# Kernel optimization log

Hardware: AMD Instinct MI355X
Metric: run time of the kernel (lower is better)

## Reference

```python
import jax, jax.numpy as jnp
import numpy as np

DIM = 192
HEADS = 6
WS = 7
N = WS * WS  # 49
B_ = 4096
NW = 64


def _relative_position_index(ws):
    coords = np.stack(np.meshgrid(np.arange(ws), np.arange(ws), indexing='ij'))  # (2, ws, ws)
    cf = coords.reshape(2, -1)  # (2, N)
    rel = cf[:, :, None] - cf[:, None, :]  # (2, N, N)
    rel = rel.transpose(1, 2, 0).copy()
    rel[:, :, 0] += ws - 1
    rel[:, :, 1] += ws - 1
    rel[:, :, 0] *= 2 * ws - 1
    return jnp.asarray(rel.sum(-1), dtype=jnp.int32)  # (N, N)


def setup_inputs() -> dict:
    key = jax.random.key(0)
    ks = jax.random.split(key, 8)
    x = jax.random.normal(ks[0], (B_, N, DIM), dtype=jnp.float32)
    mask = jax.random.normal(ks[1], (NW, N, N), dtype=jnp.float32)
    qkv_w = jax.random.normal(ks[2], (3 * DIM, DIM), dtype=jnp.float32) * 0.02
    qkv_b = jnp.zeros((3 * DIM,), dtype=jnp.float32)
    proj_w = jax.random.normal(ks[3], (DIM, DIM), dtype=jnp.float32) * 0.02
    proj_b = jnp.zeros((DIM,), dtype=jnp.float32)
    n_bias = (2 * WS - 1) * (2 * WS - 1)  # 169
    bias_table = jax.random.truncated_normal(ks[4], -2.0, 2.0, (n_bias, HEADS), dtype=jnp.float32) * 0.02
    rel_idx = _relative_position_index(WS)
    return {"x": x, "mask": mask, "qkv_w": qkv_w, "qkv_b": qkv_b,
            "proj_w": proj_w, "proj_b": proj_b, "bias_table": bias_table,
            "rel_idx": rel_idx}


def reference(x, mask, qkv_w, qkv_b, proj_w, proj_b, bias_table, rel_idx):
    Bw, n, c = x.shape
    hd = c // HEADS
    scale = hd ** -0.5
    qkv = x @ qkv_w.T + qkv_b  # (B_, N, 3C)
    qkv = qkv.reshape(Bw, n, 3, HEADS, hd).transpose(2, 0, 3, 1, 4)  # (3, B_, H, N, hd)
    q, k, v = qkv[0] * scale, qkv[1], qkv[2]
    attn = jnp.einsum('bhqd,bhkd->bhqk', q, k)  # (B_, H, N, N)
    bias = bias_table[rel_idx.reshape(-1)].reshape(n, n, HEADS).transpose(2, 0, 1)  # (H, N, N)
    attn = attn + bias[None]
    nW = mask.shape[0]
    attn = attn.reshape(Bw // nW, nW, HEADS, n, n) + mask[None, :, None]
    attn = jax.nn.softmax(attn.reshape(Bw, HEADS, n, n), axis=-1)
    out = jnp.einsum('bhqk,bhkd->bhqd', attn, v)  # (B_, H, N, hd)
    out = out.transpose(0, 2, 1, 3).reshape(Bw, n, c)
    return out @ proj_w.T + proj_b
```

## Files before the change

### kernel.cpp

```cpp
#include <hip/hip_runtime.h>
#include <hip/hip_fp16.h>


typedef short bf16x8 __attribute__((ext_vector_type(8)));
typedef float f32x4 __attribute__((ext_vector_type(4)));

#define MFMA16(a, b, c) __builtin_amdgcn_mfma_f32_16x16x32_bf16((a), (b), (c), 0, 0, 0)

#define DIMC 192
#define NTOK 49

__device__ __forceinline__ unsigned short f2bf(float f) {
  unsigned int u = __float_as_uint(f);
  u += 0x7fffu + ((u >> 16) & 1u);
  return (unsigned short)(u >> 16);
}

__device__ __forceinline__ unsigned int cvt_pk_bf16(float lo, float hi) {
  unsigned int r;
  asm("v_cvt_pk_bf16_f32 %0, %1, %2" : "=v"(r) : "v"(lo), "v"(hi));
  return r;
}

__global__ void prep_kernel(const float* __restrict__ qkv_w,
                            const float* __restrict__ proj_w,
                            const float* __restrict__ bias_table,
                            const int* __restrict__ rel_idx,
                            const float* __restrict__ mask,
                            unsigned short* __restrict__ qkv_wb,
                            unsigned short* __restrict__ proj_wb,
                            __half* __restrict__ bmT) {
  int i = blockIdx.x * 256 + threadIdx.x;
  if (i < 576 * 192) qkv_wb[i] = f2bf(qkv_w[i]);
  if (i < 192 * 192) proj_wb[i] = f2bf(proj_w[i]);
  {
    int r = i & 3;
    int q = (i >> 2) & 63;
    int lq = (i >> 8) & 3;
    int nt = (i >> 10) & 3;
    int hw = i >> 12;
    int h = hw % 6;
    int widx = hw / 6;
    int k = nt * 16 + lq * 4 + r;
    float v;
    if (k >= NTOK) v = -30000.f;
    else if (q >= NTOK) v = 0.f;
    else v = bias_table[rel_idx[q * NTOK + k] * 6 + h] +
             mask[(size_t)widx * (NTOK * NTOK) + q * NTOK + k];
    bmT[i] = __float2half(v);
  }
}

__global__ __launch_bounds__(256, 2) void winattn_kernel(
    const float* __restrict__ x,
    const float* __restrict__ qkv_b,
    const float* __restrict__ proj_b,
    const unsigned short* __restrict__ qkv_wb,
    const unsigned short* __restrict__ proj_wb,
    const __half* __restrict__ bmT,
    float* __restrict__ out) {
  __shared__ unsigned short pool[39424];
  unsigned short* xb   = pool;
  unsigned short* Qall = pool;
  unsigned short* Kall = pool + 12800;
  unsigned short* Vta  = pool + 25600;

  const int tid = threadIdx.x;
  const int b = blockIdx.x;
  const int widx = b & 63;
  const int lane = tid & 63;
  const int wv = tid >> 6;
  const int lq = lane >> 4;
  const int ln = lane & 15;

  {
    const float4* xp = (const float4*)(x + (size_t)b * (NTOK * DIMC));
    for (int i = tid; i < NTOK * DIMC / 4; i += 256) {
      float4 v = xp[i];
      int fl = i * 4;
      int r = fl / DIMC;
      int c = fl - r * DIMC;
      unsigned int lo = (unsigned int)f2bf(v.x) | ((unsigned int)f2bf(v.y) << 16);
      unsigned int hi = (unsigned int)f2bf(v.z) | ((unsigned int)f2bf(v.w) << 16);
      *(uint2*)(&xb[r * 200 + c]) = make_uint2(lo, hi);
    }
    for (int i = tid; i < 15 * 200 / 2; i += 256)
      ((unsigned int*)(&xb[49 * 200]))[i] = 0u;
  }
  __syncthreads();

  bf16x8 af[4][6];
#pragma unroll
  for (int mt = 0; mt < 4; ++mt)
#pragma unroll
    for (int ks = 0; ks < 6; ++ks)
      af[mt][ks] = *(const bf16x8*)&xb[(mt * 16 + ln) * 200 + ks * 32 + lq * 8];
  __syncthreads();

  const float scale = 0.17677669529663687f;

  for (int i = 0; i < 9; ++i) {
    int nt = wv * 9 + i;
    int c = nt * 16 + ln;
    const unsigned short* wp = qkv_wb + (size_t)c * DIMC + lq * 8;
    bf16x8 wf[6];
#pragma unroll
    for (int ks = 0; ks < 6; ++ks) wf[ks] = *(const bf16x8*)(wp + ks * 32);
    float bv = qkv_b[c];
    f32x4 a0 = (f32x4){bv, bv, bv, bv};
    f32x4 a1 = a0, a2 = a0, a3 = a0;
#pragma unroll
    for (int ks = 0; ks < 6; ++ks) {
      a0 = MFMA16(af[0][ks], wf[ks], a0);
      a1 = MFMA16(af[1][ks], wf[ks], a1);
      a2 = MFMA16(af[2][ks], wf[ks], a2);
      a3 = MFMA16(af[3][ks], wf[ks], a3);
    }
    f32x4 acc[4] = {a0, a1, a2, a3};
    int which = nt / 12;
    int colq = c - which * 192;
    if (which == 0) {
#pragma unroll
      for (int mt = 0; mt < 4; ++mt) {
        int row0 = mt * 16 + lq * 4;
#pragma unroll
        for (int r = 0; r < 4; ++r)
          Qall[(row0 + r) * 200 + colq] = f2bf(acc[mt][r] * scale);
      }
    } else if (which == 1) {
#pragma unroll
      for (int mt = 0; mt < 4; ++mt) {
        int row0 = mt * 16 + lq * 4;
#pragma unroll
        for (int r = 0; r < 4; ++r)
          Kall[(row0 + r) * 200 + colq] = f2bf(acc[mt][r]);
      }
    } else {
#pragma unroll
      for (int mt = 0; mt < 4; ++mt) {
        int row0 = mt * 16 + lq * 4;
        unsigned int lo = cvt_pk_bf16(acc[mt][0], acc[mt][1]);
        unsigned int hi = cvt_pk_bf16(acc[mt][2], acc[mt][3]);
        *(uint2*)(&Vta[colq * 72 + row0]) = make_uint2(lo, hi);
      }
    }
  }
  __syncthreads();

  f32x4 pacc[12];
#pragma unroll
  for (int nti = 0; nti < 12; ++nti) {
    float pbv = proj_b[nti * 16 + ln];
    pacc[nti] = (f32x4){pbv, pbv, pbv, pbv};
  }

  const __half* bmp = bmT + (size_t)widx * 6 * 4096;
  const int sA = ((lq & 1) << 5) | ln;
  const int sB = sA + 16;
  const int hiSel = lq >> 1;

  for (int h = 0; h < 6; ++h) {
    uint2 bmu[4];
    {
      const __half* bmh = bmp + (size_t)h * 4096;
#pragma unroll
      for (int nt = 0; nt < 4; ++nt)
        bmu[nt] = *(const uint2*)(bmh + ((nt * 4 + lq) * 64 + wv * 16 + ln) * 4);
    }

    bf16x8 qf = *(const bf16x8*)&Qall[(wv * 16 + ln) * 200 + h * 32 + lq * 8];
    f32x4 sv[4];
#pragma unroll
    for (int nt = 0; nt < 4; ++nt) {
      bf16x8 kf = *(const bf16x8*)&Kall[(nt * 16 + ln) * 200 + h * 32 + lq * 8];
      sv[nt] = MFMA16(kf, qf, ((f32x4){0.f, 0.f, 0.f, 0.f}));
    }
    float tt[4][4];
#pragma unroll
    for (int nt = 0; nt < 4; ++nt) {
      float2 f01 = __half22float2(*(const __half2*)&bmu[nt].x);
      float2 f23 = __half22float2(*(const __half2*)&bmu[nt].y);
      tt[nt][0] = sv[nt][0] + f01.x;
      tt[nt][1] = sv[nt][1] + f01.y;
      tt[nt][2] = sv[nt][2] + f23.x;
      tt[nt][3] = sv[nt][3] + f23.y;
    }
    float m = tt[0][0];
#pragma unroll
    for (int nt = 0; nt < 4; ++nt)
#pragma unroll
      for (int r = 0; r < 4; ++r) m = fmaxf(m, tt[nt][r]);
    m = fmaxf(m, __shfl_xor(m, 16, 64));
    m = fmaxf(m, __shfl_xor(m, 32, 64));
    float sum = 0.f;
#pragma unroll
    for (int nt = 0; nt < 4; ++nt)
#pragma unroll
      for (int r = 0; r < 4; ++r) {
        float e = __expf(tt[nt][r] - m);
        tt[nt][r] = e;
        sum += e;
      }
    sum += __shfl_xor(sum, 16, 64);
    sum += __shfl_xor(sum, 32, 64);
    float pinv = 1.f / sum;

    unsigned int pk[4][2];
#pragma unroll
    for (int nt = 0; nt < 4; ++nt) {
      pk[nt][0] = cvt_pk_bf16(tt[nt][0], tt[nt][1]);
      pk[nt][1] = cvt_pk_bf16(tt[nt][2], tt[nt][3]);
    }
    union U8 { unsigned int u[4]; bf16x8 v; };
    U8 pb0, pb1;
#pragma unroll
    for (int w = 0; w < 4; ++w) {
      int src = (w & 2) ? sB : sA;
      int a0 = __shfl((int)pk[0][w & 1], src, 64);
      int a1 = __shfl((int)pk[1][w & 1], src, 64);
      int b0 = __shfl((int)pk[2][w & 1], src, 64);
      int b1 = __shfl((int)pk[3][w & 1], src, 64);
      pb0.u[w] = (unsigned int)(hiSel ? a1 : a0);
      pb1.u[w] = (unsigned int)(hiSel ? b1 : b0);
    }
    f32x4 o[2];
#pragma unroll
    for (int db = 0; db < 2; ++db) {
      bf16x8 v0 = *(const bf16x8*)&Vta[(h * 32 + db * 16 + ln) * 72 + lq * 8];
      bf16x8 v1 = *(const bf16x8*)&Vta[(h * 32 + db * 16 + ln) * 72 + 32 + lq * 8];
      f32x4 acc = (f32x4){0.f, 0.f, 0.f, 0.f};
      acc = MFMA16(v0, pb0.v, acc);
      acc = MFMA16(v1, pb1.v, acc);
      o[db] = acc;
    }
    unsigned int pkO[2][2];
#pragma unroll
    for (int db = 0; db < 2; ++db) {
      pkO[db][0] = cvt_pk_bf16(o[db][0] * pinv, o[db][1] * pinv);
      pkO[db][1] = cvt_pk_bf16(o[db][2] * pinv, o[db][3] * pinv);
    }
    U8 oa;
#pragma unroll
    for (int w = 0; w < 4; ++w) {
      int src = (w & 2) ? sB : sA;
      int a0 = __shfl((int)pkO[0][w & 1], src, 64);
      int a1 = __shfl((int)pkO[1][w & 1], src, 64);
      oa.u[w] = (unsigned int)(hiSel ? a1 : a0);
    }
#pragma unroll
    for (int nti = 0; nti < 12; ++nti) {
      bf16x8 w = *(const bf16x8*)(proj_wb + (size_t)(nti * 16 + ln) * DIMC + h * 32 + lq * 8);
      pacc[nti] = MFMA16(oa.v, w, pacc[nti]);
    }
  }

  {
    float* outp = out + (size_t)b * (NTOK * DIMC);
#pragma unroll
    for (int nti = 0; nti < 12; ++nti) {
      int col = nti * 16 + ln;
#pragma unroll
      for (int r = 0; r < 4; ++r) {
        int row = wv * 16 + lq * 4 + r;
        if (row < NTOK) outp[row * DIMC + col] = pacc[nti][r];
      }
    }
  }
}

extern "C" void kernel_launch(void* const* d_in, const int* in_sizes, int n_in,
                              void* d_out, int out_size, void* d_ws, size_t ws_size,
                              hipStream_t stream) {
  const float* x = (const float*)d_in[0];
  const float* mask = (const float*)d_in[1];
  const float* qkv_w = (const float*)d_in[2];
  const float* qkv_b = (const float*)d_in[3];
  const float* proj_w = (const float*)d_in[4];
  const float* proj_b = (const float*)d_in[5];
  const float* bias_table = (const float*)d_in[6];
  const int* rel_idx = (const int*)d_in[7];

  unsigned short* qkv_wb = (unsigned short*)d_ws;
  unsigned short* proj_wb = qkv_wb + 576 * 192;
  __half* bmT = (__half*)(proj_wb + 192 * 192);

  prep_kernel<<<6144, 256, 0, stream>>>(qkv_w, proj_w, bias_table, rel_idx,
                                        mask, qkv_wb, proj_wb, bmT);
  winattn_kernel<<<4096, 256, 0, stream>>>(x, qkv_b, proj_b,
                                           qkv_wb, proj_wb, bmT,
                                           (float*)d_out);
}
```

Before: 528.3 us.

## Split heads across 8 waves, keep Q in registers, use exp2 softmax

Doubles the block to 512 threads (8 waves). Each pair of waves shares a 16-row strip and splits the six heads three and three, and the two partial projection results are combined through shared memory before the store. Q is computed per wave straight into MFMA operand registers, which removes the Q buffer from LDS and cuts shared memory per block. Softmax uses exp2 with log2e folded into the Q scale and the precomputed bias/mask. The aim is more parallelism and occupancy, at the cost of an extra reduction through LDS, an extra barrier and more register pressure.

```diff
diff --git a/kernel.cpp b/kernel.cpp
--- a/kernel.cpp
+++ b/kernel.cpp
@@ -30,6 +30,7 @@
                             unsigned short* __restrict__ qkv_wb,
                             unsigned short* __restrict__ proj_wb,
                             __half* __restrict__ bmT) {
+  const float LOG2E = 1.4426950408889634f;
   int i = blockIdx.x * 256 + threadIdx.x;
   if (i < 576 * 192) qkv_wb[i] = f2bf(qkv_w[i]);
   if (i < 192 * 192) proj_wb[i] = f2bf(proj_w[i]);
@@ -43,15 +44,15 @@
     int widx = hw / 6;
     int k = nt * 16 + lq * 4 + r;
     float v;
-    if (k >= NTOK) v = -30000.f;
+    if (k >= NTOK) v = -30000.f * LOG2E;
     else if (q >= NTOK) v = 0.f;
-    else v = bias_table[rel_idx[q * NTOK + k] * 6 + h] +
-             mask[(size_t)widx * (NTOK * NTOK) + q * NTOK + k];
+    else v = (bias_table[rel_idx[q * NTOK + k] * 6 + h] +
+              mask[(size_t)widx * (NTOK * NTOK) + q * NTOK + k]) * LOG2E;
     bmT[i] = __float2half(v);
   }
 }
 
-__global__ __launch_bounds__(256, 2) void winattn_kernel(
+__global__ __launch_bounds__(512, 6) void winattn_kernel(
     const float* __restrict__ x,
     const float* __restrict__ qkv_b,
     const float* __restrict__ proj_b,
@@ -59,11 +60,11 @@
     const unsigned short* __restrict__ proj_wb,
     const __half* __restrict__ bmT,
     float* __restrict__ out) {
-  __shared__ unsigned short pool[39424];
+  __shared__ unsigned short pool[26624];
   unsigned short* xb   = pool;
-  unsigned short* Qall = pool;
-  unsigned short* Kall = pool + 12800;
-  unsigned short* Vta  = pool + 25600;
+  unsigned short* Kall = pool;
+  unsigned short* Vta  = pool + 12800;
+  float* scr = (float*)pool;
 
   const int tid = threadIdx.x;
   const int b = blockIdx.x;
@@ -72,10 +73,12 @@
   const int wv = tid >> 6;
   const int lq = lane >> 4;
   const int ln = lane & 15;
+  const int strip = wv >> 1;
+  const int hsel = wv & 1;
 
   {
     const float4* xp = (const float4*)(x + (size_t)b * (NTOK * DIMC));
-    for (int i = tid; i < NTOK * DIMC / 4; i += 256) {
+    for (int i = tid; i < NTOK * DIMC / 4; i += 512) {
       float4 v = xp[i];
       int fl = i * 4;
       int r = fl / DIMC;
@@ -84,7 +87,7 @@
       unsigned int hi = (unsigned int)f2bf(v.z) | ((unsigned int)f2bf(v.w) << 16);
       *(uint2*)(&xb[r * 200 + c]) = make_uint2(lo, hi);
     }
-    for (int i = tid; i < 15 * 200 / 2; i += 256)
+    for (int i = tid; i < 15 * 200 / 2; i += 512)
       ((unsigned int*)(&xb[49 * 200]))[i] = 0u;
   }
   __syncthreads();
@@ -95,18 +98,54 @@
 #pragma unroll
     for (int ks = 0; ks < 6; ++ks)
       af[mt][ks] = *(const bf16x8*)&xb[(mt * 16 + ln) * 200 + ks * 32 + lq * 8];
-  __syncthreads();
-
-  const float scale = 0.17677669529663687f;
-
-  for (int i = 0; i < 9; ++i) {
-    int nt = wv * 9 + i;
-    int c = nt * 16 + ln;
-    const unsigned short* wp = qkv_wb + (size_t)c * DIMC + lq * 8;
+  bf16x8 afs[6];
+#pragma unroll
+  for (int ks = 0; ks < 6; ++ks)
+    afs[ks] = *(const bf16x8*)&xb[(strip * 16 + ln) * 200 + ks * 32 + lq * 8];
+  __syncthreads();
+
+  const float scale2 = 0.17677669529663687f * 1.4426950408889634f;
+  const int sA = ((lq & 1) << 5) | ln;
+  const int sB = sA + 16;
+  const int hiSel = lq >> 1;
+  union U8 { unsigned int u[4]; bf16x8 v; };
+
+  unsigned int pkQ[6][2];
+  const int dbase = hsel * 96;
+#pragma unroll
+  for (int ct = 0; ct < 6; ++ct) {
+    const unsigned short* wp = qkv_wb + (size_t)(dbase + ct * 16 + ln) * DIMC + lq * 8;
     bf16x8 wf[6];
 #pragma unroll
     for (int ks = 0; ks < 6; ++ks) wf[ks] = *(const bf16x8*)(wp + ks * 32);
-    float bv = qkv_b[c];
+    float4 bq = *(const float4*)&qkv_b[dbase + ct * 16 + lq * 4];
+    f32x4 acc = (f32x4){bq.x, bq.y, bq.z, bq.w};
+#pragma unroll
+    for (int ks = 0; ks < 6; ++ks) acc = MFMA16(wf[ks], afs[ks], acc);
+    pkQ[ct][0] = cvt_pk_bf16(acc[0] * scale2, acc[1] * scale2);
+    pkQ[ct][1] = cvt_pk_bf16(acc[2] * scale2, acc[3] * scale2);
+  }
+  U8 qb[3];
+#pragma unroll
+  for (int hh = 0; hh < 3; ++hh)
+#pragma unroll
+    for (int w = 0; w < 4; ++w) {
+      int src = (w & 2) ? sB : sA;
+      int a0 = __shfl((int)pkQ[2 * hh][w & 1], src, 64);
+      int a1 = __shfl((int)pkQ[2 * hh + 1][w & 1], src, 64);
+      qb[hh].u[w] = (unsigned int)(hiSel ? a1 : a0);
+    }
+
+  for (int i = 0; i < 3; ++i) {
+    int t = wv * 3 + i;
+    int isK = (t < 12);
+    int colt = isK ? t : (t - 12);
+    int row = (isK ? 192 : 384) + colt * 16 + ln;
+    const unsigned short* wp = qkv_wb + (size_t)row * DIMC + lq * 8;
+    bf16x8 wf[6];
+#pragma unroll
+    for (int ks = 0; ks < 6; ++ks) wf[ks] = *(const bf16x8*)(wp + ks * 32);
+    float bv = qkv_b[row];
     f32x4 a0 = (f32x4){bv, bv, bv, bv};
     f32x4 a1 = a0, a2 = a0, a3 = a0;
 #pragma unroll
@@ -117,23 +156,14 @@
       a3 = MFMA16(af[3][ks], wf[ks], a3);
     }
     f32x4 acc[4] = {a0, a1, a2, a3};
-    int which = nt / 12;
-    int colq = c - which * 192;
-    if (which == 0) {
+    int db = colt * 16 + ln;
+    if (isK) {
 #pragma unroll
       for (int mt = 0; mt < 4; ++mt) {
         int row0 = mt * 16 + lq * 4;
 #pragma unroll
         for (int r = 0; r < 4; ++r)
-          Qall[(row0 + r) * 200 + colq] = f2bf(acc[mt][r] * scale);
-      }
-    } else if (which == 1) {
-#pragma unroll
-      for (int mt = 0; mt < 4; ++mt) {
-        int row0 = mt * 16 + lq * 4;
-#pragma unroll
-        for (int r = 0; r < 4; ++r)
-          Kall[(row0 + r) * 200 + colq] = f2bf(acc[mt][r]);
+          Kall[(row0 + r) * 200 + db] = f2bf(acc[mt][r]);
       }
     } else {
 #pragma unroll
@@ -141,7 +171,7 @@
         int row0 = mt * 16 + lq * 4;
         unsigned int lo = cvt_pk_bf16(acc[mt][0], acc[mt][1]);
         unsigned int hi = cvt_pk_bf16(acc[mt][2], acc[mt][3]);
-        *(uint2*)(&Vta[colq * 72 + row0]) = make_uint2(lo, hi);
+        *(uint2*)(&Vta[db * 72 + row0]) = make_uint2(lo, hi);
       }
     }
   }
@@ -150,30 +180,27 @@
   f32x4 pacc[12];
 #pragma unroll
   for (int nti = 0; nti < 12; ++nti) {
-    float pbv = proj_b[nti * 16 + ln];
+    float pbv = hsel ? 0.f : proj_b[nti * 16 + ln];
     pacc[nti] = (f32x4){pbv, pbv, pbv, pbv};
   }
 
   const __half* bmp = bmT + (size_t)widx * 6 * 4096;
-  const int sA = ((lq & 1) << 5) | ln;
-  const int sB = sA + 16;
-  const int hiSel = lq >> 1;
-
-  for (int h = 0; h < 6; ++h) {
+
+  for (int hh = 0; hh < 3; ++hh) {
+    const int h = hsel * 3 + hh;
     uint2 bmu[4];
     {
       const __half* bmh = bmp + (size_t)h * 4096;
 #pragma unroll
       for (int nt = 0; nt < 4; ++nt)
-        bmu[nt] = *(const uint2*)(bmh + ((nt * 4 + lq) * 64 + wv * 16 + ln) * 4);
-    }
-
-    bf16x8 qf = *(const bf16x8*)&Qall[(wv * 16 + ln) * 200 + h * 32 + lq * 8];
+        bmu[nt] = *(const uint2*)(bmh + ((nt * 4 + lq) * 64 + strip * 16 + ln) * 4);
+    }
+
     f32x4 sv[4];
 #pragma unroll
     for (int nt = 0; nt < 4; ++nt) {
       bf16x8 kf = *(const bf16x8*)&Kall[(nt * 16 + ln) * 200 + h * 32 + lq * 8];
-      sv[nt] = MFMA16(kf, qf, ((f32x4){0.f, 0.f, 0.f, 0.f}));
+      sv[nt] = MFMA16(kf, qb[hh].v, ((f32x4){0.f, 0.f, 0.f, 0.f}));
     }
     float tt[4][4];
 #pragma unroll
@@ -185,22 +212,24 @@
       tt[nt][2] = sv[nt][2] + f23.x;
       tt[nt][3] = sv[nt][3] + f23.y;
     }
-    float m = tt[0][0];
-#pragma unroll
-    for (int nt = 0; nt < 4; ++nt)
-#pragma unroll
-      for (int r = 0; r < 4; ++r) m = fmaxf(m, tt[nt][r]);
+    float m0 = fmaxf(fmaxf(tt[0][0], tt[0][1]), fmaxf(tt[0][2], tt[0][3]));
+    float m1 = fmaxf(fmaxf(tt[1][0], tt[1][1]), fmaxf(tt[1][2], tt[1][3]));
+    float m2 = fmaxf(fmaxf(tt[2][0], tt[2][1]), fmaxf(tt[2][2], tt[2][3]));
+    float m3 = fmaxf(fmaxf(tt[3][0], tt[3][1]), fmaxf(tt[3][2], tt[3][3]));
+    float m = fmaxf(fmaxf(m0, m1), fmaxf(m2, m3));
     m = fmaxf(m, __shfl_xor(m, 16, 64));
     m = fmaxf(m, __shfl_xor(m, 32, 64));
-    float sum = 0.f;
-#pragma unroll
-    for (int nt = 0; nt < 4; ++nt)
-#pragma unroll
-      for (int r = 0; r < 4; ++r) {
-        float e = __expf(tt[nt][r] - m);
-        tt[nt][r] = e;
-        sum += e;
-      }
+    float s[4];
+#pragma unroll
+    for (int nt = 0; nt < 4; ++nt) {
+      float e0 = exp2f(tt[nt][0] - m);
+      float e1 = exp2f(tt[nt][1] - m);
+      float e2 = exp2f(tt[nt][2] - m);
+      float e3 = exp2f(tt[nt][3] - m);
+      tt[nt][0] = e0; tt[nt][1] = e1; tt[nt][2] = e2; tt[nt][3] = e3;
+      s[nt] = (e0 + e1) + (e2 + e3);
+    }
+    float sum = (s[0] + s[1]) + (s[2] + s[3]);
     sum += __shfl_xor(sum, 16, 64);
     sum += __shfl_xor(sum, 32, 64);
     float pinv = 1.f / sum;
@@ -211,7 +240,6 @@
       pk[nt][0] = cvt_pk_bf16(tt[nt][0], tt[nt][1]);
       pk[nt][1] = cvt_pk_bf16(tt[nt][2], tt[nt][3]);
     }
-    union U8 { unsigned int u[4]; bf16x8 v; };
     U8 pb0, pb1;
 #pragma unroll
     for (int w = 0; w < 4; ++w) {
@@ -249,20 +277,33 @@
     }
 #pragma unroll
     for (int nti = 0; nti < 12; ++nti) {
-      bf16x8 w = *(const bf16x8*)(proj_wb + (size_t)(nti * 16 + ln) * DIMC + h * 32 + lq * 8);
+      bf16x8 w = *(const bf16x8*)(proj_wb +
+          (size_t)(nti * 16 + ln) * DIMC + h * 32 + lq * 8);
       pacc[nti] = MFMA16(oa.v, w, pacc[nti]);
     }
   }
 
-  {
+  __syncthreads();
+  if (hsel) {
+    float* sp = scr + strip * (16 * 196);
+#pragma unroll
+    for (int nti = 0; nti < 12; ++nti)
+#pragma unroll
+      for (int r = 0; r < 4; ++r)
+        sp[(lq * 4 + r) * 196 + nti * 16 + ln] = pacc[nti][r];
+  }
+  __syncthreads();
+  if (!hsel) {
     float* outp = out + (size_t)b * (NTOK * DIMC);
+    const float* sp = scr + strip * (16 * 196);
 #pragma unroll
     for (int nti = 0; nti < 12; ++nti) {
       int col = nti * 16 + ln;
 #pragma unroll
       for (int r = 0; r < 4; ++r) {
-        int row = wv * 16 + lq * 4 + r;
-        if (row < NTOK) outp[row * DIMC + col] = pacc[nti][r];
+        int row = strip * 16 + lq * 4 + r;
+        if (row < NTOK)
+          outp[row * DIMC + col] = pacc[nti][r] + sp[(lq * 4 + r) * 196 + col];
       }
     }
   }
@@ -286,7 +327,7 @@
 
   prep_kernel<<<6144, 256, 0, stream>>>(qkv_w, proj_w, bias_table, rel_idx,
                                         mask, qkv_wb, proj_wb, bmT);
-  winattn_kernel<<<4096, 256, 0, stream>>>(x, qkv_b, proj_b,
+  winattn_kernel<<<4096, 512, 0, stream>>>(x, qkv_b, proj_b,
                                            qkv_wb, proj_wb, bmT,
                                            (float*)d_out);
 }
```

New measurement: 1.140 ms. +115.9%, slower.
